# Kernel optimization log

Measured on AMD Instinct MI355X. Metric: run time of the kernel, lower is better.

## Reference

```python
import jax, jax.numpy as jnp
import numpy as np

N = 50000     # num_nodes
E = 600000    # num_edges
H = 128       # h_dim
OUT = 32      # out_dim
R = 64        # num_rels
B = 16        # num_bases


def setup_inputs() -> dict:
    key = jax.random.key(0)
    ks = jax.random.split(key, 11)
    src = jax.random.randint(ks[0], (E,), 0, N)
    dst = jax.random.randint(ks[1], (E,), 0, N)
    etype = jax.random.randint(ks[2], (E,), 0, R)
    norm = jax.random.uniform(ks[3], (E, 1), dtype=jnp.float32)  # edge norm (e.g. 1/deg)
    emb = jax.random.normal(ks[4], (N, H), dtype=jnp.float32) * 0.05
    # basis-decomposed relation weights: W_r = sum_b comp[r,b] * V[b]
    V1 = jax.random.normal(ks[5], (B, H, H), dtype=jnp.float32) * (1.0 / np.sqrt(H))
    comp1 = jax.random.normal(ks[6], (R, B), dtype=jnp.float32) * (1.0 / np.sqrt(B))
    bias1 = jnp.zeros((H,), dtype=jnp.float32)
    V2 = jax.random.normal(ks[7], (B, H, OUT), dtype=jnp.float32) * (1.0 / np.sqrt(H))
    comp2 = jax.random.normal(ks[8], (R, B), dtype=jnp.float32) * (1.0 / np.sqrt(B))
    bias2 = jnp.zeros((OUT,), dtype=jnp.float32)
    return {"src": src, "dst": dst, "etype": etype, "norm": norm, "emb": emb,
            "V1": V1, "comp1": comp1, "bias1": bias1,
            "V2": V2, "comp2": comp2, "bias2": bias2}


def _rel_graph_conv(x, src, dst, etype, norm, V, comp, bias):
    # message for edge e: (x[src_e] @ W_{etype_e}) * norm_e, W_r = sum_b comp[r,b] V_b.
    # Since W is linear, fold norm into the gathered features, and aggregate
    # per (dst, basis) BEFORE the dense basis matmul (aggregate-first trick):
    #   agg[v, b] = sum_{e: dst_e=v} comp[etype_e, b] * norm_e * x[src_e]
    #   out[v]    = sum_b agg[v, b] @ V_b + bias
    xs = x[src] * norm                      # [E, in]
    w = comp[etype]                         # [E, B] per-edge basis coefficients
    # loop over the small fixed basis count (B=16), reusing the [E, in] buffer
    agg = jnp.stack(
        [jax.ops.segment_sum(xs * w[:, b:b + 1], dst, num_segments=N) for b in range(B)],
        axis=1,
    )                                       # [N, B, in]
    return jnp.einsum('nbi,bio->no', agg, V) + bias


def reference(src, dst, etype, norm, emb, V1, comp1, bias1, V2, comp2, bias2):
    h = _rel_graph_conv(emb, src, dst, etype, norm, V1, comp1, bias1)
    h = jax.nn.relu(h)                      # dropout p=0.0 -> identity
    h = _rel_graph_conv(h, src, dst, etype, norm, V2, comp2, bias2)
    return h
```

## Files before the change

kernel.cpp:

```cpp
#include <hip/hip_runtime.h>
#include <hip/hip_bf16.h>

#define NN 50000
#define EE 600000
#define HH 128
#define OUTD 32
#define RR 64
#define BB 16
#define KK 2048
#define SC_B ((NN + 1023) / 1024)

typedef short s16x8 __attribute__((ext_vector_type(8)));
typedef float f32x4 __attribute__((ext_vector_type(4)));
typedef float f32x2 __attribute__((ext_vector_type(2)));
typedef unsigned short ushort_t;
typedef unsigned int uint_t;
typedef __attribute__((address_space(3))) uint_t lds_u32;
typedef const __attribute__((address_space(1))) uint_t glb_u32;

__device__ inline ushort_t f_to_bf16(float f){
    __hip_bfloat16 h = __float2bfloat16(f);
    return *reinterpret_cast<ushort_t*>(&h);
}
__device__ inline uint_t pack_bf16x2(float a, float b){
    return (uint_t)f_to_bf16(a) | ((uint_t)f_to_bf16(b) << 16);
}

__global__ void zero_i32(int* p, int n){
    int i = blockIdx.x*256 + threadIdx.x;
    if (i < n) p[i] = 0;
}

__global__ void hist_kernel(const int* __restrict__ dst, int* counts){
    int e = blockIdx.x*256 + threadIdx.x;
    if (e < EE) atomicAdd(&counts[dst[e]], 1);
}

__global__ void scan_part(const int* __restrict__ counts, int* __restrict__ tot){
    int b = blockIdx.x, t = threadIdx.x;
    int i0 = b*1024 + t*4;
    int s = 0;
    if (i0 + 3 < NN){
        int4 v = *reinterpret_cast<const int4*>(&counts[i0]);
        s = v.x + v.y + v.z + v.w;
    } else {
        for (int j = 0; j < 4; j++) if (i0 + j < NN) s += counts[i0 + j];
    }
    #pragma unroll
    for (int off = 32; off; off >>= 1) s += __shfl_xor(s, off, 64);
    __shared__ int ws[4];
    if ((t & 63) == 0) ws[t >> 6] = s;
    __syncthreads();
    if (t == 0) tot[b] = ws[0] + ws[1] + ws[2] + ws[3];
}

__global__ void scan_tot(int* tot){
    int t = threadIdx.x;
    int v = (t < SC_B) ? tot[t] : 0;
    int x = v;
    #pragma unroll
    for (int off = 1; off < 64; off <<= 1){
        int y = __shfl_up(x, off, 64);
        if (t >= off) x += y;
    }
    if (t < SC_B) tot[t] = x - v;
}

__global__ void scan_final(const int* __restrict__ counts, const int* __restrict__ tot,
                           int* __restrict__ offsets, int* __restrict__ cursor){
    int b = blockIdx.x, t = threadIdx.x, lane = t & 63, wv = t >> 6;
    int i0 = b*1024 + t*4;
    int v[4]; int s = 0;
    #pragma unroll
    for (int j = 0; j < 4; j++){ v[j] = (i0 + j < NN) ? counts[i0 + j] : 0; s += v[j]; }
    int x = s;
    #pragma unroll
    for (int off = 1; off < 64; off <<= 1){
        int y = __shfl_up(x, off, 64);
        if (lane >= off) x += y;
    }
    __shared__ int ws[4];
    if (lane == 63) ws[wv] = x;
    __syncthreads();
    int pre = tot[b];
    for (int i = 0; i < wv; i++) pre += ws[i];
    int run = pre + x - s;
    #pragma unroll
    for (int j = 0; j < 4; j++){
        if (i0 + j < NN){
            cursor[i0 + j] = run;
            offsets[i0 + j + 1] = run + v[j];
        }
        run += v[j];
    }
    if (b == 0 && t == 0) offsets[0] = 0;
}

__global__ void scatter_kernel(const int* __restrict__ dst, const int* __restrict__ src,
                               const int* __restrict__ etype, const float* __restrict__ norm,
                               int* cursor, int* __restrict__ msrc, int* __restrict__ netn){
    int e = blockIdx.x*256 + threadIdx.x;
    if (e >= EE) return;
    int d = dst[e];
    int r = atomicAdd(&cursor[d], 1);
    msrc[r] = src[e];
    netn[r] = (__float_as_int(norm[e]) & ~63) | etype[e];
}

__global__ void convw_kernel(const float* __restrict__ V1, const float* __restrict__ V2,
                             ushort_t* __restrict__ Wt1, ushort_t* __restrict__ Wt2){
    int i = blockIdx.x*256 + threadIdx.x;
    if (i < HH*KK){
        int o = i / KK, k = i % KK;
        Wt1[i] = f_to_bf16(V1[(size_t)k*HH + o]);
    } else {
        int j = i - HH*KK;
        if (j < OUTD*KK){
            int o = j / KK, k = j % KK;
            Wt2[j] = f_to_bf16(V2[(size_t)k*OUTD + o]);
        }
    }
}

__global__ void conv_emb(const float* __restrict__ emb, ushort_t* __restrict__ xb){
    int i = blockIdx.x*256 + threadIdx.x;
    if (i < NN*HH/2){
        float2 f = *reinterpret_cast<const float2*>(emb + 2*(size_t)i);
        *reinterpret_cast<uint_t*>(xb + 2*(size_t)i) = pack_bf16x2(f.x, f.y);
    }
}

__global__ __launch_bounds__(256, 8) void agg_kernel(
    const ushort_t* __restrict__ xin, const int* __restrict__ msrc,
    const int* __restrict__ netn, const int* __restrict__ offsets,
    const float* __restrict__ comp, ushort_t* __restrict__ agg,
    int v0, int vc)
{
    int w = threadIdx.x >> 6, lane = threadIdx.x & 63;
    int v = v0 + blockIdx.x*4 + w;
    if (v >= v0 + vc) return;
    int p0 = offsets[v];
    int dd = offsets[v+1] - p0;
    const uint_t* xrow = reinterpret_cast<const uint_t*>(xin);

    f32x2 accA[8], accB[8];
    #pragma unroll
    for (int bp = 0; bp < 8; bp++){
        accA[bp].x = 0.f; accA[bp].y = 0.f;
        accB[bp].x = 0.f; accB[bp].y = 0.f;
    }

    for (int c0 = 0; c0 < dd; c0 += 64){
        int nc = min(64, dd - c0);
        int li = p0 + c0 + min(lane, nc - 1);
        int mp = msrc[li];
        int nr = netn[li];
        uint_t xr[8];
        #pragma unroll
        for (int j = 0; j < 8; ++j){
            int sr = __builtin_amdgcn_readlane(mp, min(j, nc - 1));
            xr[j] = xrow[(size_t)sr*64 + lane];
        }
        for (int eb = 0; eb < nc; eb += 8){
            #pragma unroll
            for (int j = 0; j < 8; ++j){
                int e = eb + j;
                int ec = min(e, nc - 1);
                int nb = __builtin_amdgcn_readlane(nr, ec);
                int et = nb & 63;
                float nw = (e < nc) ? __int_as_float(nb & ~63) : 0.f;
                uint_t u = xr[j];
                f32x2 xs;
                xs.x = __uint_as_float(u << 16) * nw;
                xs.y = __uint_as_float(u & 0xffff0000u) * nw;
                int en = e + 8;
                if (en < nc){
                    int srn = __builtin_amdgcn_readlane(mp, en);
                    xr[j] = xrow[(size_t)srn*64 + lane];
                }
                const f32x2* cp = reinterpret_cast<const f32x2*>(comp + et*BB);
                #pragma unroll
                for (int bp = 0; bp < 8; bp++){
                    f32x2 c2 = cp[bp];
                    asm("v_pk_fma_f32 %0, %1, %2, %0 op_sel:[0,0,0] op_sel_hi:[1,0,1]"
                        : "+v"(accA[bp]) : "s"(c2), "v"(xs));
                    asm("v_pk_fma_f32 %0, %1, %2, %0 op_sel:[0,1,0] op_sel_hi:[1,1,1]"
                        : "+v"(accB[bp]) : "s"(c2), "v"(xs));
                }
            }
        }
    }
    uint_t* arow = reinterpret_cast<uint_t*>(agg) + (size_t)(v - v0)*1024 + lane;
    #pragma unroll
    for (int b = 0; b < BB; b++)
        arow[b*64] = pack_bf16x2(accA[b>>1][b&1], accB[b>>1][b&1]);
}

template<int BN, bool RELU, bool OUT_BF16>
__global__ __launch_bounds__(512, 6) void gemm_kernel(
    const ushort_t* __restrict__ A, const ushort_t* __restrict__ Wt,
    const float* __restrict__ bias, void* __restrict__ yout, int vc)
{
    __shared__ __align__(16) char Ald[2][64*128];
    __shared__ __align__(16) char Bld[2][BN*128];
    constexpr int CT = BN / 32;
    int tid = threadIdx.x, lane = tid & 63, lane15 = lane & 15;
    int w = tid >> 6, wr = w >> 1, wc = w & 1;
    int m0 = blockIdx.x * 64;

    int sr_ = tid >> 3, sj_ = (tid & 7) ^ (sr_ & 7);
    const ushort_t* agp = A + (size_t)(m0 + min(sr_, vc - 1))*KK + sj_*8;
    const ushort_t* bgp0 = Wt + (size_t)sr_*KK + sj_*8;
    const ushort_t* bgp1 = Wt + (size_t)(64 + sr_)*KK + sj_*8;

    auto stage = [&](int buf){
        __builtin_amdgcn_global_load_lds((glb_u32*)agp,
            (lds_u32*)(&Ald[buf][w*1024]), 16, 0, 0);
        if constexpr (BN == 128){
            __builtin_amdgcn_global_load_lds((glb_u32*)bgp0,
                (lds_u32*)(&Bld[buf][w*1024]), 16, 0, 0);
            __builtin_amdgcn_global_load_lds((glb_u32*)bgp1,
                (lds_u32*)(&Bld[buf][8192 + w*1024]), 16, 0, 0);
            bgp1 += 64;
        } else {
            if (w < 4)
                __builtin_amdgcn_global_load_lds((glb_u32*)bgp0,
                    (lds_u32*)(&Bld[buf][w*1024]), 16, 0, 0);
        }
        agp += 64; bgp0 += 64;
    };

    f32x4 acc[CT];
    #pragma unroll
    for (int ct = 0; ct < CT; ct++)
        #pragma unroll
        for (int j = 0; j < 4; j++) acc[ct][j] = 0.f;

    int arow = wr*16 + lane15;
    auto compute = [&](int buf){
        #pragma unroll
        for (int ks = 0; ks < 2; ks++){
            int csw = (ks*4 + (lane >> 4)) ^ (lane15 & 7);
            s16x8 a = *reinterpret_cast<const s16x8*>(&Ald[buf][arow*128 + csw*16]);
            #pragma unroll
            for (int ct = 0; ct < CT; ct++){
                int brow = wc*(BN/2) + ct*16 + lane15;
                s16x8 b = *reinterpret_cast<const s16x8*>(&Bld[buf][brow*128 + csw*16]);
                acc[ct] = __builtin_amdgcn_mfma_f32_16x16x32_bf16(a, b, acc[ct], 0,0,0);
            }
        }
    };

    stage(0);
    __syncthreads();
    for (int t = 0; t < KK/64; t += 2){
        if (t + 1 < KK/64) stage(1);
        compute(0);
        __syncthreads();
        if (t + 2 < KK/64) stage(0);
        compute(1);
        __syncthreads();
    }

    int rb = m0 + wr*16 + ((lane >> 4) << 2);
    #pragma unroll
    for (int ct = 0; ct < CT; ct++){
        int col = wc*(BN/2) + ct*16 + lane15;
        float bv = bias[col];
        #pragma unroll
        for (int r = 0; r < 4; r++){
            int row = rb + r;
            if (row < vc){
                float val = acc[ct][r] + bv;
                if (RELU) val = fmaxf(val, 0.f);
                if (OUT_BF16)
                    reinterpret_cast<ushort_t*>(yout)[(size_t)row*BN + col] = f_to_bf16(val);
                else
                    reinterpret_cast<float*>(yout)[(size_t)row*BN + col] = val;
            }
        }
    }
}

extern "C" void kernel_launch(void* const* d_in, const int* in_sizes, int n_in,
                              void* d_out, int out_size, void* d_ws, size_t ws_size,
                              hipStream_t stream){
    const int*   src   = (const int*)d_in[0];
    const int*   dst   = (const int*)d_in[1];
    const int*   etype = (const int*)d_in[2];
    const float* norm  = (const float*)d_in[3];
    const float* emb   = (const float*)d_in[4];
    const float* V1    = (const float*)d_in[5];
    const float* comp1 = (const float*)d_in[6];
    const float* bias1 = (const float*)d_in[7];
    const float* V2    = (const float*)d_in[8];
    const float* comp2 = (const float*)d_in[9];
    const float* bias2 = (const float*)d_in[10];
    float* out = (float*)d_out;

    char* w = (char*)d_ws;
    auto alloc = [&](size_t bytes) -> char* {
        char* p = w; w += (bytes + 255) & ~(size_t)255; return p;
    };
    int*      offsets = (int*)alloc((NN + 1) * 4);
    int*      counts  = (int*)alloc(NN * 4);
    int*      cursor  = (int*)alloc(NN * 4);
    int*      tot     = (int*)alloc(SC_B * 4);
    int*      msrc    = (int*)alloc((size_t)EE * 4);
    int*      netn    = (int*)alloc((size_t)EE * 4);
    ushort_t* Wt1     = (ushort_t*)alloc((size_t)HH * KK * 2);
    ushort_t* Wt2     = (ushort_t*)alloc((size_t)OUTD * KK * 2);
    ushort_t* xb      = (ushort_t*)alloc((size_t)NN * HH * 2);
    ushort_t* h       = (ushort_t*)alloc((size_t)NN * HH * 2);
    size_t used  = (size_t)(w - (char*)d_ws);
    size_t avail = ws_size > used ? ws_size - used : 0;
    int chunkN = (int)(avail / ((size_t)KK * 2));
    chunkN &= ~63;
    if (chunkN < 64) chunkN = 64;
    if (chunkN > NN) chunkN = NN;
    ushort_t* agg = (ushort_t*)w;

    zero_i32<<<(NN + 255)/256, 256, 0, stream>>>(counts, NN);
    hist_kernel<<<(EE + 255)/256, 256, 0, stream>>>(dst, counts);
    scan_part<<<SC_B, 256, 0, stream>>>(counts, tot);
    scan_tot<<<1, 64, 0, stream>>>(tot);
    scan_final<<<SC_B, 256, 0, stream>>>(counts, tot, offsets, cursor);
    scatter_kernel<<<(EE + 255)/256, 256, 0, stream>>>(dst, src, etype, norm,
                                                       cursor, msrc, netn);
    convw_kernel<<<((HH + OUTD)*KK + 255)/256, 256, 0, stream>>>(V1, V2, Wt1, Wt2);
    conv_emb<<<(NN*HH/2 + 255)/256, 256, 0, stream>>>(emb, xb);

    for (int v0 = 0; v0 < NN; v0 += chunkN){
        int vc = (NN - v0 < chunkN) ? (NN - v0) : chunkN;
        agg_kernel<<<(vc + 3)/4, 256, 0, stream>>>(
            xb, msrc, netn, offsets, comp1, agg, v0, vc);
        gemm_kernel<HH, true, true><<<(vc + 63)/64, 512, 0, stream>>>(
            agg, Wt1, bias1, h + (size_t)v0 * HH, vc);
    }
    for (int v0 = 0; v0 < NN; v0 += chunkN){
        int vc = (NN - v0 < chunkN) ? (NN - v0) : chunkN;
        agg_kernel<<<(vc + 3)/4, 256, 0, stream>>>(
            h, msrc, netn, offsets, comp2, agg, v0, vc);
        gemm_kernel<OUTD, false, false><<<(vc + 63)/64, 512, 0, stream>>>(
            agg, Wt2, bias2, out + (size_t)v0 * OUTD, vc);
    }
}
```

Before: 319.1 us.

## Enlarge GEMM M-tile to 128 rows and switch to single-barrier vmcnt pipelining

The basis GEMM kernel now processes 128 rows per block instead of 64. Each wave computes a 32x64 (or 16x32) sub-tile, so weight tiles loaded into LDS are reused across more rows. The double-buffer loop is restructured to issue the next stage's async global-to-LDS loads, then wait only on the previous stage with s_waitcnt vmcnt before the barrier, which overlaps loads with compute. The trade-off is more LDS and registers per block (launch bounds drop to 4) and fewer blocks.

```diff
diff --git a/kernel.cpp b/kernel.cpp
--- a/kernel.cpp
+++ b/kernel.cpp
@@ -197,86 +197,118 @@
 }
 
 template<int BN, bool RELU, bool OUT_BF16>
-__global__ __launch_bounds__(512, 6) void gemm_kernel(
+__global__ __launch_bounds__(512, 4) void gemm_kernel(
     const ushort_t* __restrict__ A, const ushort_t* __restrict__ Wt,
     const float* __restrict__ bias, void* __restrict__ yout, int vc)
 {
-    __shared__ __align__(16) char Ald[2][64*128];
+    __shared__ __align__(16) char Ald[2][128*128];
     __shared__ __align__(16) char Bld[2][BN*128];
-    constexpr int CT = BN / 32;
+    constexpr int RT = (BN == 128) ? 2 : 1;
+    constexpr int CT = (BN == 128) ? 4 : 2;
+    constexpr int NT = KK / 64;
     int tid = threadIdx.x, lane = tid & 63, lane15 = lane & 15;
-    int w = tid >> 6, wr = w >> 1, wc = w & 1;
-    int m0 = blockIdx.x * 64;
-
-    int sr_ = tid >> 3, sj_ = (tid & 7) ^ (sr_ & 7);
-    const ushort_t* agp = A + (size_t)(m0 + min(sr_, vc - 1))*KK + sj_*8;
-    const ushort_t* bgp0 = Wt + (size_t)sr_*KK + sj_*8;
-    const ushort_t* bgp1 = Wt + (size_t)(64 + sr_)*KK + sj_*8;
+    int w = tid >> 6;
+    int wrbase = (BN == 128) ? (w >> 1)*32 : w*16;
+    int wcbase = (BN == 128) ? (w & 1)*64 : 0;
+    int m0 = blockIdx.x * 128;
+
+    int rl = lane >> 3, jl = lane & 7;
+    int ra0 = w*2*8 + rl,  ra1 = (w*2+1)*8 + rl;
+    const ushort_t* agp0 = A + (size_t)(m0 + min(ra0, vc-1))*KK + ((jl ^ (ra0 & 7))*8);
+    const ushort_t* agp1 = A + (size_t)(m0 + min(ra1, vc-1))*KK + ((jl ^ (ra1 & 7))*8);
+    const ushort_t* bgp0;
+    const ushort_t* bgp1;
+    if (BN == 128){
+        bgp0 = Wt + (size_t)ra0*KK + ((jl ^ (ra0 & 7))*8);
+        bgp1 = Wt + (size_t)ra1*KK + ((jl ^ (ra1 & 7))*8);
+    } else {
+        int rb = w*8 + rl;
+        bgp0 = Wt + (size_t)min(rb, BN-1)*KK + ((jl ^ (rb & 7))*8);
+        bgp1 = nullptr;
+    }
 
     auto stage = [&](int buf){
-        __builtin_amdgcn_global_load_lds((glb_u32*)agp,
-            (lds_u32*)(&Ald[buf][w*1024]), 16, 0, 0);
+        __builtin_amdgcn_global_load_lds((glb_u32*)agp0,
+            (lds_u32*)(&Ald[buf][(w*2+0)*1024]), 16, 0, 0);
+        __builtin_amdgcn_global_load_lds((glb_u32*)agp1,
+            (lds_u32*)(&Ald[buf][(w*2+1)*1024]), 16, 0, 0);
+        agp0 += 64; agp1 += 64;
         if constexpr (BN == 128){
             __builtin_amdgcn_global_load_lds((glb_u32*)bgp0,
-                (lds_u32*)(&Bld[buf][w*1024]), 16, 0, 0);
+                (lds_u32*)(&Bld[buf][(w*2+0)*1024]), 16, 0, 0);
             __builtin_amdgcn_global_load_lds((glb_u32*)bgp1,
-                (lds_u32*)(&Bld[buf][8192 + w*1024]), 16, 0, 0);
-            bgp1 += 64;
+                (lds_u32*)(&Bld[buf][(w*2+1)*1024]), 16, 0, 0);
+            bgp0 += 64; bgp1 += 64;
         } else {
-            if (w < 4)
+            if (w < 4){
                 __builtin_amdgcn_global_load_lds((glb_u32*)bgp0,
                     (lds_u32*)(&Bld[buf][w*1024]), 16, 0, 0);
-        }
-        agp += 64; bgp0 += 64;
+                bgp0 += 64;
+            }
+        }
     };
 
-    f32x4 acc[CT];
-    #pragma unroll
-    for (int ct = 0; ct < CT; ct++)
+    f32x4 acc[RT][CT];
+    #pragma unroll
+    for (int t = 0; t < RT; t++)
         #pragma unroll
-        for (int j = 0; j < 4; j++) acc[ct][j] = 0.f;
-
-    int arow = wr*16 + lane15;
+        for (int ct = 0; ct < CT; ct++)
+            #pragma unroll
+            for (int j = 0; j < 4; j++) acc[t][ct][j] = 0.f;
+
     auto compute = [&](int buf){
         #pragma unroll
         for (int ks = 0; ks < 2; ks++){
             int csw = (ks*4 + (lane >> 4)) ^ (lane15 & 7);
-            s16x8 a = *reinterpret_cast<const s16x8*>(&Ald[buf][arow*128 + csw*16]);
             #pragma unroll
-            for (int ct = 0; ct < CT; ct++){
-                int brow = wc*(BN/2) + ct*16 + lane15;
-                s16x8 b = *reinterpret_cast<const s16x8*>(&Bld[buf][brow*128 + csw*16]);
-                acc[ct] = __builtin_amdgcn_mfma_f32_16x16x32_bf16(a, b, acc[ct], 0,0,0);
+            for (int t = 0; t < RT; t++){
+                int arow = wrbase + t*16 + lane15;
+                s16x8 a = *reinterpret_cast<const s16x8*>(&Ald[buf][arow*128 + csw*16]);
+                #pragma unroll
+                for (int ct = 0; ct < CT; ct++){
+                    int brow = wcbase + ct*16 + lane15;
+                    s16x8 b = *reinterpret_cast<const s16x8*>(&Bld[buf][brow*128 + csw*16]);
+                    acc[t][ct] = __builtin_amdgcn_mfma_f32_16x16x32_bf16(a, b, acc[t][ct], 0,0,0);
+                }
             }
         }
     };
 
     stage(0);
-    __syncthreads();
-    for (int t = 0; t < KK/64; t += 2){
-        if (t + 1 < KK/64) stage(1);
-        compute(0);
-        __syncthreads();
-        if (t + 2 < KK/64) stage(0);
-        compute(1);
-        __syncthreads();
-    }
-
-    int rb = m0 + wr*16 + ((lane >> 4) << 2);
-    #pragma unroll
-    for (int ct = 0; ct < CT; ct++){
-        int col = wc*(BN/2) + ct*16 + lane15;
-        float bv = bias[col];
+    for (int t = 0; t < NT; ++t){
+        int cur = t & 1;
+        if (t + 1 < NT){
+            stage(cur ^ 1);
+            if (BN == 128)       asm volatile("s_waitcnt vmcnt(4)" ::: "memory");
+            else if (w < 4)      asm volatile("s_waitcnt vmcnt(3)" ::: "memory");
+            else                 asm volatile("s_waitcnt vmcnt(2)" ::: "memory");
+        } else {
+            asm volatile("s_waitcnt vmcnt(0)" ::: "memory");
+        }
+        __builtin_amdgcn_s_barrier();
+        __builtin_amdgcn_sched_barrier(0);
+        compute(cur);
+        __builtin_amdgcn_s_barrier();
+    }
+
+    #pragma unroll
+    for (int t = 0; t < RT; t++){
+        int rb = m0 + wrbase + t*16 + ((lane >> 4) << 2);
         #pragma unroll
-        for (int r = 0; r < 4; r++){
-            int row = rb + r;
-            if (row < vc){
-                float val = acc[ct][r] + bv;
-                if (RELU) val = fmaxf(val, 0.f);
-                if (OUT_BF16)
-                    reinterpret_cast<ushort_t*>(yout)[(size_t)row*BN + col] = f_to_bf16(val);
-                else
-                    reinterpret_cast<float*>(yout)[(size_t)row*BN + col] = val;
+        for (int ct = 0; ct < CT; ct++){
+            int col = wcbase + ct*16 + lane15;
+            float bv = bias[col];
+            #pragma unroll
+            for (int r = 0; r < 4; r++){
+                int row = rb + r;
+                if (row < vc){
+                    float val = acc[t][ct][r] + bv;
+                    if (RELU) val = fmaxf(val, 0.f);
+                    if (OUT_BF16)
+                        reinterpret_cast<ushort_t*>(yout)[(size_t)row*BN + col] = f_to_bf16(val);
+                    else
+                        reinterpret_cast<float*>(yout)[(size_t)row*BN + col] = val;
+                }
             }
         }
     }
@@ -315,8 +347,8 @@
     size_t used  = (size_t)(w - (char*)d_ws);
     size_t avail = ws_size > used ? ws_size - used : 0;
     int chunkN = (int)(avail / ((size_t)KK * 2));
-    chunkN &= ~63;
-    if (chunkN < 64) chunkN = 64;
+    chunkN &= ~127;
+    if (chunkN < 128) chunkN = 128;
     if (chunkN > NN) chunkN = NN;
     ushort_t* agg = (ushort_t*)w;
 
@@ -334,14 +366,14 @@
         int vc = (NN - v0 < chunkN) ? (NN - v0) : chunkN;
         agg_kernel<<<(vc + 3)/4, 256, 0, stream>>>(
             xb, msrc, netn, offsets, comp1, agg, v0, vc);
-        gemm_kernel<HH, true, true><<<(vc + 63)/64, 512, 0, stream>>>(
+        gemm_kernel<HH, true, true><<<(vc + 127)/128, 512, 0, stream>>>(
             agg, Wt1, bias1, h + (size_t)v0 * HH, vc);
     }
     for (int v0 = 0; v0 < NN; v0 += chunkN){
         int vc = (NN - v0 < chunkN) ? (NN - v0) : chunkN;
         agg_kernel<<<(vc + 3)/4, 256, 0, stream>>>(
             h, msrc, netn, offsets, comp2, agg, v0, vc);
-        gemm_kernel<OUTD, false, false><<<(vc + 63)/64, 512, 0, stream>>>(
+        gemm_kernel<OUTD, false, false><<<(vc + 127)/128, 512, 0, stream>>>(
             agg, Wt2, bias2, out + (size_t)v0 * OUTD, vc);
     }
 }
```

New measurement: 310.1 us. -2.8%, faster.
